# Kernel optimization log

Measured on AMD Instinct MI355X. Metric: run time of the kernel, lower is better.

The kernel has to match this reference:

```python
import jax, jax.numpy as jnp
import numpy as np

IOU_THRESH = 0.1
TEACHER_CONF = 0.2
EPS = 1e-7


def box_iou(box1, box2, giou=False):
    # box1: [B,m,4], box2: [B,n,4] in cxcywh -> pairwise IoU [B,m,n]
    b1 = box1[:, :, None, :]  # [B,m,1,4]
    b2 = box2[:, None, :, :]  # [B,1,n,4]
    x1, y1, w1, h1 = b1[..., 0], b1[..., 1], b1[..., 2], b1[..., 3]
    x2, y2, w2, h2 = b2[..., 0], b2[..., 1], b2[..., 2], b2[..., 3]
    b1x1, b1x2, b1y1, b1y2 = x1 - w1 / 2, x1 + w1 / 2, y1 - h1 / 2, y1 + h1 / 2
    b2x1, b2x2, b2y1, b2y2 = x2 - w2 / 2, x2 + w2 / 2, y2 - h2 / 2, y2 + h2 / 2
    inter = (jnp.maximum(jnp.minimum(b1x2, b2x2) - jnp.maximum(b1x1, b2x1), 0.0)
             * jnp.maximum(jnp.minimum(b1y2, b2y2) - jnp.maximum(b1y1, b2y1), 0.0))
    union = w1 * h1 + w2 * h2 - inter + EPS
    iou = inter / union
    if giou:
        c_area = ((jnp.maximum(b1x2, b2x2) - jnp.minimum(b1x1, b2x1))
                  * (jnp.maximum(b1y2, b2y2) - jnp.minimum(b1y1, b2y1)) + EPS)
        return iou - (c_area - union) / c_area
    return iou


def setup_inputs() -> dict:
    key = jax.random.key(0)
    k1, k2, k3, k4 = jax.random.split(key, 4)
    B, Q, C = 16, 900, 80
    return {
        "s_pred_logits": jax.random.normal(k1, (B, Q, C), dtype=jnp.float32),
        "s_pred_boxes": jax.random.uniform(k2, (B, Q, 4), dtype=jnp.float32),
        "t_pred_logits": jax.random.normal(k3, (B, Q, C), dtype=jnp.float32),
        "t_pred_boxes": jax.random.uniform(k4, (B, Q, 4), dtype=jnp.float32),
        "target_nums": 128,
    }


def reference(s_pred_logits, s_pred_boxes, t_pred_logits, t_pred_boxes, target_nums):
    B, Q, C = s_pred_logits.shape
    tn = jnp.asarray(target_nums, dtype=s_pred_logits.dtype)

    # teacher confidence flag (detached in original; bool => no grad anyway)
    conf = jax.nn.sigmoid(t_pred_logits).max(-1) > TEACHER_CONF  # [B,Q]

    # pairwise IoU and best-teacher match per student query
    iou = box_iou(s_pred_boxes, t_pred_boxes)        # [B,Q,Q]
    max_iou = iou.max(-1)                            # [B,Q]
    max_idx = jnp.argmax(iou, -1)                    # [B,Q]

    # torch: gather((max_iou>th).repeat & conf_flag, 1, idx[...,None]) reads column 0
    flag = jnp.take_along_axis(max_iou > IOU_THRESH, max_idx, axis=1) & conf[:, 0:1]  # [B,Q]

    # torch gathers column 0 of the pairwise L1 / GIoU matrices -> only t_boxes[:,0] matters
    l1_col0 = jnp.abs(s_pred_boxes - t_pred_boxes[:, 0:1, :]).sum(-1)               # [B,Q]
    giou_col0 = 1.0 - box_iou(s_pred_boxes, t_pred_boxes[:, 0:1, :], giou=True)[:, :, 0]  # [B,Q]
    l1_g = jnp.take_along_axis(l1_col0, max_idx, axis=1)
    giou_g = jnp.take_along_axis(giou_col0, max_idx, axis=1)

    lbox_l1 = jnp.where(flag, l1_g, 0.0).sum() / tn * 5.0
    lbox_iou = jnp.where(flag, giou_g, 0.0).sum() / tn * 2.0

    # pairwise BCE over flattened [B*Q] rows; torch gather picks column max_idx_flat[p]
    # (indexes rows 0..Q-1 of the flattened teacher -- faithfully reproduced)
    s_flat = s_pred_logits.reshape(B * Q, C)
    t_flat = t_pred_logits.reshape(B * Q, C)
    idx_flat = max_idx.reshape(-1)                   # values in [0,Q)
    t_probs = jax.nn.sigmoid(t_flat[idx_flat])       # [B*Q, C]
    # BCEWithLogits(x, t) = softplus(x) - x*t  (stable)
    bce = jax.nn.softplus(s_flat) - s_flat * t_probs
    lcls = bce.mean(-1).sum() / tn

    loss = lbox_l1 + lbox_iou + lcls
    return jnp.where(conf.any(), loss, 0.0)
```

## Files before the change

### kernel.cpp

```cpp
#include <hip/hip_runtime.h>
#include <math.h>

#define NB 16
#define NQ 900
#define NQP 928
#define NC 80
#define EPSV 1e-7f
#define IOU_THR 0.1f
#define SPB 8
#define CHB 113
#define NBLK (NB * CHB)

__device__ __forceinline__ float sigm(float x) { return 1.0f / (1.0f + __expf(-x)); }

__global__ __launch_bounds__(256) void k_main(
    const float* __restrict__ s_logits,
    const float* __restrict__ s_boxes,
    const float* __restrict__ t_logits,
    const float* __restrict__ t_boxes,
    int*    __restrict__ g_cnt,
    float*  __restrict__ g_v,
    float2* __restrict__ g_part)
{
    __shared__ float4 tcor[NQP];
    __shared__ float  tarea[NQP];
    __shared__ int    lidx[SPB];
    __shared__ float  sconf0;
    __shared__ float2 sres[SPB];

    const int bx  = blockIdx.x;
    const int b   = blockIdx.y;
    const int tid = threadIdx.x;

    if (tid < SPB) sres[tid] = make_float2(0.f, 0.f);

    const float4* tb = (const float4*)(t_boxes + b * NQ * 4);
    for (int i = tid; i < NQP; i += 256) {
        if (i < NQ) {
            float4 t = tb[i];
            float hw = t.z * 0.5f, hh = t.w * 0.5f;
            tcor[i]  = make_float4(t.x - hw, t.x + hw, t.y - hh, t.y + hh);
            tarea[i] = t.z * t.w;
        } else {
            tcor[i]  = make_float4(2e9f, -2e9f, 2e9f, -2e9f);
            tarea[i] = 1.0f;
        }
    }
    if (tid < 64) {
        const float* tl = t_logits + b * NQ * NC;
        float m = tl[tid];
        if (tid < NC - 64) m = fmaxf(m, tl[tid + 64]);
        for (int s = 32; s >= 1; s >>= 1) m = fmaxf(m, __shfl_xor(m, s, 64));
        if (tid == 0) sconf0 = (sigm(m) > 0.2f) ? 1.0f : 0.0f;
    }
    __syncthreads();

    const int s  = tid >> 5;
    const int tc = tid & 31;
    const int sq = bx * SPB + s;
    const bool act = (sq < NQ);
    float best = -1.0f; int bidx = 0;
    float4 sb = make_float4(0.f, 0.f, 0.f, 0.f);
    float sx1 = 0.f, sx2 = 0.f, sy1 = 0.f, sy2 = 0.f, sarea = 0.f;
    if (act) {
        sb = ((const float4*)(s_boxes + b * NQ * 4))[sq];
        float shw = sb.z * 0.5f, shh = sb.w * 0.5f;
        sx1 = sb.x - shw; sx2 = sb.x + shw;
        sy1 = sb.y - shh; sy2 = sb.y + shh;
        sarea = sb.z * sb.w;
        #pragma unroll 4
        for (int i = 0; i < 29; ++i) {
            int t = tc + (i << 5);
            float4 c = tcor[t];
            float iw = fminf(sx2, c.y) - fmaxf(sx1, c.x);
            float ih = fminf(sy2, c.w) - fmaxf(sy1, c.z);
            float inter = fmaxf(iw, 0.0f) * fmaxf(ih, 0.0f);
            float uni = sarea + tarea[t] - inter + EPSV;
            float iou = inter * __frcp_rn(uni);
            if (iou > best) { best = iou; bidx = t; }
        }
    }
    for (int m = 1; m <= 16; m <<= 1) {
        float ov = __shfl_xor(best, m, 64);
        int   oi = __shfl_xor(bidx, m, 64);
        if (ov > best || (ov == best && oi < bidx)) { best = ov; bidx = oi; }
    }
    if (act && tc == 0) {
        int o = b * NQ + sq;
        lidx[s] = bidx;
        atomicAdd(&g_cnt[b * NQ + bidx], 1);
        float4 t0 = tb[0];
        float4 c  = tcor[0];
        float iw = fminf(sx2, c.y) - fmaxf(sx1, c.x);
        float ih = fminf(sy2, c.w) - fmaxf(sy1, c.z);
        float inter = fmaxf(iw, 0.0f) * fmaxf(ih, 0.0f);
        float uni = sarea + tarea[0] - inter + EPSV;
        float iou = inter / uni;
        float cw = fmaxf(sx2, c.y) - fminf(sx1, c.x);
        float ch = fmaxf(sy2, c.w) - fminf(sy1, c.z);
        float carea = cw * ch + EPSV;
        float giou1 = 1.0f - (iou - (carea - uni) / carea);
        float l1 = fabsf(sb.x - t0.x) + fabsf(sb.y - t0.y) +
                   fabsf(sb.z - t0.z) + fabsf(sb.w - t0.w);
        float v = 0.0f;
        if (sconf0 > 0.0f && best > IOU_THR) v = 5.0f * l1 + 2.0f * giou1;
        g_v[o] = v;
    }
    __syncthreads();

    const int wv  = tid >> 6, lane = tid & 63;
    const int grp = lane >> 4, tc2 = lane & 15;
    const int r   = wv * 4 + grp;
    const int sq2 = bx * SPB + r;
    if (r < SPB && sq2 < NQ) {
        int row = b * NQ + sq2;
        int j   = lidx[r];
        const float* srow = s_logits + row * NC;
        const float* trow = t_logits + row * NC;
        const float* grow = t_logits + j * NC;
        float4 svv = *(const float4*)(srow + tc2 * 4);
        float4 tvv = *(const float4*)(trow + tc2 * 4);
        float4 gvv = *(const float4*)(grow + tc2 * 4);
        float  s4 = srow[64 + tc2];
        float  t4 = trow[64 + tc2];
        float  g4 = grow[64 + tc2];
        float bce = 0.f;
        {
            float se[5] = {svv.x, svv.y, svv.z, svv.w, s4};
            float ge[5] = {gvv.x, gvv.y, gvv.z, gvv.w, g4};
            #pragma unroll
            for (int e = 0; e < 5; ++e) {
                float s0 = se[e], g0 = ge[e];
                bce += fmaxf(s0, 0.f) + __logf(1.0f + __expf(-fabsf(s0)))
                     - s0 * __builtin_amdgcn_rcpf(1.0f + __expf(-g0));
            }
        }
        float tmax = fmaxf(fmaxf(fmaxf(tvv.x, tvv.y), fmaxf(tvv.z, tvv.w)), t4);
        for (int m = 8; m >= 1; m >>= 1) {
            bce  += __shfl_xor(bce, m, 64);
            tmax  = fmaxf(tmax, __shfl_xor(tmax, m, 64));
        }
        if (tc2 == 0)
            sres[r] = make_float2(bce * (1.0f / (float)NC),
                                  (sigm(tmax) > 0.2f) ? 1.0f : 0.0f);
    }
    __syncthreads();
    if (tid < 64) {
        float bs = 0.f, ca = 0.f;
        if (tid < SPB) { float2 p = sres[tid]; bs = p.x; ca = p.y; }
        for (int m = 32; m >= 1; m >>= 1) {
            bs += __shfl_xor(bs, m, 64);
            ca  = fmaxf(ca, __shfl_xor(ca, m, 64));
        }
        if (tid == 0) g_part[b * CHB + bx] = make_float2(bs, ca);
    }
}

__global__ __launch_bounds__(1024) void k_final(
    const int*    __restrict__ g_cnt,
    const float*  __restrict__ g_v,
    const float2* __restrict__ g_part,
    const int*    __restrict__ tn_p,
    float* __restrict__ out)
{
    const int tid = threadIdx.x;
    float bs = 0.f, ca = 0.f;
    for (int i = tid; i < NBLK; i += 1024) {
        float2 p = g_part[i];
        bs += p.x; ca = fmaxf(ca, p.y);
    }
    float vs = 0.f;
    #pragma unroll
    for (int k = 0; k < 15; ++k) {
        int i = tid + k * 1024;
        if (i < NB * NQ) vs += (float)g_cnt[i] * g_v[i];
    }
    __shared__ float rb[16], rv[16], rc[16];
    const int wv = tid >> 6, lane = tid & 63;
    for (int m = 32; m >= 1; m >>= 1) {
        bs += __shfl_xor(bs, m, 64);
        vs += __shfl_xor(vs, m, 64);
        ca  = fmaxf(ca, __shfl_xor(ca, m, 64));
    }
    if (lane == 0) { rb[wv] = bs; rv[wv] = vs; rc[wv] = ca; }
    __syncthreads();
    if (tid == 0) {
        float sb = 0.f, sv = 0.f, sc = 0.f;
        for (int k = 0; k < 16; ++k) { sb += rb[k]; sv += rv[k]; sc = fmaxf(sc, rc[k]); }
        float tn = (float)tn_p[0];
        out[0] = (sc > 0.f) ? (sv + sb) / tn : 0.0f;
    }
}

extern "C" void kernel_launch(void* const* d_in, const int* in_sizes, int n_in,
                              void* d_out, int out_size, void* d_ws, size_t ws_size,
                              hipStream_t stream) {
    const float* s_logits = (const float*)d_in[0];
    const float* s_boxes  = (const float*)d_in[1];
    const float* t_logits = (const float*)d_in[2];
    const float* t_boxes  = (const float*)d_in[3];
    const int*   tn       = (const int*)d_in[4];
    float* out = (float*)d_out;

    char* ws = (char*)d_ws;
    int*    g_cnt  = (int*)(ws);
    float*  g_v    = (float*)(ws + 57600);
    float2* g_part = (float2*)(ws + 115200);

    hipMemsetAsync(g_cnt, 0, NB * NQ * sizeof(int), stream);
    k_main<<<dim3(CHB, NB), 256, 0, stream>>>(s_logits, s_boxes, t_logits, t_boxes,
                                              g_cnt, g_v, g_part);
    k_final<<<1, 1024, 0, stream>>>(g_cnt, g_v, g_part, tn, out);
}
```

Measured before the change: 30.56 us.

## Process 64 student queries per block with per-lane IoU scan over teacher quarters

Restructures the main kernel so each block handles 64 student queries instead of 8. Each lane owns one student box and each wave scans a quarter of the teacher boxes, keeping four independent running maxima. Partial argmaxes are merged through shared memory instead of warp shuffles. This amortises the per-block teacher-box staging and conf0 computation over 8x more queries, cutting redundant global loads and the block count from 1808 to 240. The cost is fewer blocks to occupy the GPU, and LDS reads of tcor are now wave-uniform broadcasts rather than strided accesses.

```diff
diff --git a/kernel.cpp b/kernel.cpp
--- a/kernel.cpp
+++ b/kernel.cpp
@@ -3,12 +3,13 @@
 
 #define NB 16
 #define NQ 900
-#define NQP 928
+#define NQP 912
+#define PPH 228
 #define NC 80
 #define EPSV 1e-7f
 #define IOU_THR 0.1f
-#define SPB 8
-#define CHB 113
+#define SPB 64
+#define CHB 15
 #define NBLK (NB * CHB)
 
 __device__ __forceinline__ float sigm(float x) { return 1.0f / (1.0f + __expf(-x)); }
@@ -24,6 +25,8 @@
 {
     __shared__ float4 tcor[NQP];
     __shared__ float  tarea[NQP];
+    __shared__ float  candv[4][SPB];
+    __shared__ int    candi[4][SPB];
     __shared__ int    lidx[SPB];
     __shared__ float  sconf0;
     __shared__ float2 sres[SPB];
@@ -31,6 +34,7 @@
     const int bx  = blockIdx.x;
     const int b   = blockIdx.y;
     const int tid = threadIdx.x;
+    const int wv  = tid >> 6, lane = tid & 63;
 
     if (tid < SPB) sres[tid] = make_float2(0.f, 0.f);
 
@@ -55,99 +59,116 @@
     }
     __syncthreads();
 
-    const int s  = tid >> 5;
-    const int tc = tid & 31;
-    const int sq = bx * SPB + s;
+    const int sq  = bx * SPB + lane;
     const bool act = (sq < NQ);
-    float best = -1.0f; int bidx = 0;
     float4 sb = make_float4(0.f, 0.f, 0.f, 0.f);
-    float sx1 = 0.f, sx2 = 0.f, sy1 = 0.f, sy2 = 0.f, sarea = 0.f;
-    if (act) {
-        sb = ((const float4*)(s_boxes + b * NQ * 4))[sq];
-        float shw = sb.z * 0.5f, shh = sb.w * 0.5f;
-        sx1 = sb.x - shw; sx2 = sb.x + shw;
-        sy1 = sb.y - shh; sy2 = sb.y + shh;
-        sarea = sb.z * sb.w;
-        #pragma unroll 4
-        for (int i = 0; i < 29; ++i) {
-            int t = tc + (i << 5);
-            float4 c = tcor[t];
+    if (act) sb = ((const float4*)(s_boxes + b * NQ * 4))[sq];
+    const float shw = sb.z * 0.5f, shh = sb.w * 0.5f;
+    const float sx1 = sb.x - shw, sx2 = sb.x + shw;
+    const float sy1 = sb.y - shh, sy2 = sb.y + shh;
+    const float sarea = sb.z * sb.w;
+
+    float bv0 = -1.f, bv1 = -1.f, bv2 = -1.f, bv3 = -1.f;
+    int   bi0 = 0,    bi1 = 0,    bi2 = 0,    bi3 = 0;
+    const int tb0 = wv * PPH;
+#define IOU_STEP(T, BV, BI)                                                    \
+    {                                                                          \
+        float4 c = tcor[(T)];                                                  \
+        float iw = fminf(sx2, c.y) - fmaxf(sx1, c.x);                          \
+        float ih = fminf(sy2, c.w) - fmaxf(sy1, c.z);                          \
+        float inter = fmaxf(iw, 0.0f) * fmaxf(ih, 0.0f);                       \
+        float uni = sarea + tarea[(T)] - inter + EPSV;                         \
+        float iou = inter * __frcp_rn(uni);                                    \
+        if (iou > BV) { BV = iou; BI = (T); }                                  \
+    }
+    for (int i = 0; i < PPH; i += 4) {
+        int t = tb0 + i;
+        IOU_STEP(t + 0, bv0, bi0)
+        IOU_STEP(t + 1, bv1, bi1)
+        IOU_STEP(t + 2, bv2, bi2)
+        IOU_STEP(t + 3, bv3, bi3)
+    }
+#undef IOU_STEP
+    float best = bv0; int bidx = bi0;
+    if (bv1 > best || (bv1 == best && bi1 < bidx)) { best = bv1; bidx = bi1; }
+    if (bv2 > best || (bv2 == best && bi2 < bidx)) { best = bv2; bidx = bi2; }
+    if (bv3 > best || (bv3 == best && bi3 < bidx)) { best = bv3; bidx = bi3; }
+    candv[wv][lane] = best; candi[wv][lane] = bidx;
+    __syncthreads();
+
+    if (wv == 0) {
+        float bst = candv[0][lane]; int bix = candi[0][lane];
+        #pragma unroll
+        for (int p = 1; p < 4; ++p) {
+            float ov = candv[p][lane]; int oi = candi[p][lane];
+            if (ov > bst || (ov == bst && oi < bix)) { bst = ov; bix = oi; }
+        }
+        if (act) {
+            int o = b * NQ + sq;
+            lidx[lane] = bix;
+            atomicAdd(&g_cnt[b * NQ + bix], 1);
+            float4 t0 = tb[0];
+            float4 c  = tcor[0];
             float iw = fminf(sx2, c.y) - fmaxf(sx1, c.x);
             float ih = fminf(sy2, c.w) - fmaxf(sy1, c.z);
             float inter = fmaxf(iw, 0.0f) * fmaxf(ih, 0.0f);
-            float uni = sarea + tarea[t] - inter + EPSV;
-            float iou = inter * __frcp_rn(uni);
-            if (iou > best) { best = iou; bidx = t; }
-        }
-    }
-    for (int m = 1; m <= 16; m <<= 1) {
-        float ov = __shfl_xor(best, m, 64);
-        int   oi = __shfl_xor(bidx, m, 64);
-        if (ov > best || (ov == best && oi < bidx)) { best = ov; bidx = oi; }
-    }
-    if (act && tc == 0) {
-        int o = b * NQ + sq;
-        lidx[s] = bidx;
-        atomicAdd(&g_cnt[b * NQ + bidx], 1);
-        float4 t0 = tb[0];
-        float4 c  = tcor[0];
-        float iw = fminf(sx2, c.y) - fmaxf(sx1, c.x);
-        float ih = fminf(sy2, c.w) - fmaxf(sy1, c.z);
-        float inter = fmaxf(iw, 0.0f) * fmaxf(ih, 0.0f);
-        float uni = sarea + tarea[0] - inter + EPSV;
-        float iou = inter / uni;
-        float cw = fmaxf(sx2, c.y) - fminf(sx1, c.x);
-        float ch = fmaxf(sy2, c.w) - fminf(sy1, c.z);
-        float carea = cw * ch + EPSV;
-        float giou1 = 1.0f - (iou - (carea - uni) / carea);
-        float l1 = fabsf(sb.x - t0.x) + fabsf(sb.y - t0.y) +
-                   fabsf(sb.z - t0.z) + fabsf(sb.w - t0.w);
-        float v = 0.0f;
-        if (sconf0 > 0.0f && best > IOU_THR) v = 5.0f * l1 + 2.0f * giou1;
-        g_v[o] = v;
-    }
-    __syncthreads();
-
-    const int wv  = tid >> 6, lane = tid & 63;
+            float uni = sarea + tarea[0] - inter + EPSV;
+            float iou = inter / uni;
+            float cw = fmaxf(sx2, c.y) - fminf(sx1, c.x);
+            float ch = fmaxf(sy2, c.w) - fminf(sy1, c.z);
+            float carea = cw * ch + EPSV;
+            float giou1 = 1.0f - (iou - (carea - uni) / carea);
+            float l1 = fabsf(sb.x - t0.x) + fabsf(sb.y - t0.y) +
+                       fabsf(sb.z - t0.z) + fabsf(sb.w - t0.w);
+            float v = 0.0f;
+            if (sconf0 > 0.0f && bst > IOU_THR) v = 5.0f * l1 + 2.0f * giou1;
+            g_v[o] = v;
+        }
+    }
+    __syncthreads();
+
     const int grp = lane >> 4, tc2 = lane & 15;
-    const int r   = wv * 4 + grp;
-    const int sq2 = bx * SPB + r;
-    if (r < SPB && sq2 < NQ) {
-        int row = b * NQ + sq2;
-        int j   = lidx[r];
-        const float* srow = s_logits + row * NC;
-        const float* trow = t_logits + row * NC;
-        const float* grow = t_logits + j * NC;
-        float4 svv = *(const float4*)(srow + tc2 * 4);
-        float4 tvv = *(const float4*)(trow + tc2 * 4);
-        float4 gvv = *(const float4*)(grow + tc2 * 4);
-        float  s4 = srow[64 + tc2];
-        float  t4 = trow[64 + tc2];
-        float  g4 = grow[64 + tc2];
-        float bce = 0.f;
-        {
-            float se[5] = {svv.x, svv.y, svv.z, svv.w, s4};
-            float ge[5] = {gvv.x, gvv.y, gvv.z, gvv.w, g4};
-            #pragma unroll
-            for (int e = 0; e < 5; ++e) {
-                float s0 = se[e], g0 = ge[e];
-                bce += fmaxf(s0, 0.f) + __logf(1.0f + __expf(-fabsf(s0)))
-                     - s0 * __builtin_amdgcn_rcpf(1.0f + __expf(-g0));
+    #pragma unroll
+    for (int p = 0; p < 4; ++p) {
+        const int r   = p * 16 + wv * 4 + grp;
+        const int sq2 = bx * SPB + r;
+        if (sq2 < NQ) {
+            int row = b * NQ + sq2;
+            int j   = lidx[r];
+            const float* srow = s_logits + row * NC;
+            const float* trow = t_logits + row * NC;
+            const float* grow = t_logits + j * NC;
+            float4 svv = *(const float4*)(srow + tc2 * 4);
+            float4 tvv = *(const float4*)(trow + tc2 * 4);
+            float4 gvv = *(const float4*)(grow + tc2 * 4);
+            float  s4 = srow[64 + tc2];
+            float  t4 = trow[64 + tc2];
+            float  g4 = grow[64 + tc2];
+            float bce = 0.f;
+            {
+                float se[5] = {svv.x, svv.y, svv.z, svv.w, s4};
+                float ge[5] = {gvv.x, gvv.y, gvv.z, gvv.w, g4};
+                #pragma unroll
+                for (int e = 0; e < 5; ++e) {
+                    float s0 = se[e], g0 = ge[e];
+                    bce += fmaxf(s0, 0.f) + __logf(1.0f + __expf(-fabsf(s0)))
+                         - s0 * __builtin_amdgcn_rcpf(1.0f + __expf(-g0));
+                }
             }
-        }
-        float tmax = fmaxf(fmaxf(fmaxf(tvv.x, tvv.y), fmaxf(tvv.z, tvv.w)), t4);
-        for (int m = 8; m >= 1; m >>= 1) {
-            bce  += __shfl_xor(bce, m, 64);
-            tmax  = fmaxf(tmax, __shfl_xor(tmax, m, 64));
-        }
-        if (tc2 == 0)
-            sres[r] = make_float2(bce * (1.0f / (float)NC),
-                                  (sigm(tmax) > 0.2f) ? 1.0f : 0.0f);
+            float tmax = fmaxf(fmaxf(fmaxf(tvv.x, tvv.y), fmaxf(tvv.z, tvv.w)), t4);
+            for (int m = 8; m >= 1; m >>= 1) {
+                bce  += __shfl_xor(bce, m, 64);
+                tmax  = fmaxf(tmax, __shfl_xor(tmax, m, 64));
+            }
+            if (tc2 == 0)
+                sres[r] = make_float2(bce * (1.0f / (float)NC),
+                                      (sigm(tmax) > 0.2f) ? 1.0f : 0.0f);
+        }
     }
     __syncthreads();
     if (tid < 64) {
-        float bs = 0.f, ca = 0.f;
-        if (tid < SPB) { float2 p = sres[tid]; bs = p.x; ca = p.y; }
+        float2 pr = sres[tid];
+        float bs = pr.x, ca = pr.y;
         for (int m = 32; m >= 1; m >>= 1) {
             bs += __shfl_xor(bs, m, 64);
             ca  = fmaxf(ca, __shfl_xor(ca, m, 64));
@@ -165,10 +186,7 @@
 {
     const int tid = threadIdx.x;
     float bs = 0.f, ca = 0.f;
-    for (int i = tid; i < NBLK; i += 1024) {
-        float2 p = g_part[i];
-        bs += p.x; ca = fmaxf(ca, p.y);
-    }
+    if (tid < NBLK) { float2 p = g_part[tid]; bs = p.x; ca = p.y; }
     float vs = 0.f;
     #pragma unroll
     for (int k = 0; k < 15; ++k) {
```

Result: slower. 35.94 us (+17.6%).
